# Optimization experiments

Hardware: AMD Instinct MI355X
Metric: run time of the kernel (lower is better)

## Reference

```python
import jax, jax.numpy as jnp
import numpy as np

N, E, C, A, F = 10000, 128000, 128, 10, 8
LDIMS = (1, 3, 5)  # 0e, 1o, 2e spherical-harmonic block sizes
NPATH = len(LDIMS)


def setup_inputs() -> dict:
    key = jax.random.key(0)
    ks = jax.random.split(key, 16)
    rn = lambda k, s, sc=1.0: jax.random.normal(k, s, dtype=jnp.float32) * sc
    inp = {
        "node_attrs": rn(ks[0], (N, A)),
        "node_feats": rn(ks[1], (N, C)),
        "edge_attrs_real": rn(ks[2], (E, 9)),
        "edge_attrs_imag": rn(ks[3], (E, 9)),
        "edge_feats": jax.random.uniform(ks[4], (E, F), dtype=jnp.float32),
        "edge_index": jax.random.randint(ks[5], (2, E), 0, N, dtype=jnp.int32),
        # learned parameters (e3nn 1/sqrt(fan_in) normalization folded into init)
        "W_up": rn(ks[6], (C, C), 1.0 / np.sqrt(C)),            # o3.Linear on 128x0e
        "W_skip": rn(ks[7], (C, A, C), 1.0 / np.sqrt(C * A)),    # FullyConnectedTensorProduct
        "W_mlp1": rn(ks[8], (F, 64), 1.0 / np.sqrt(F)),
        "W_mlp2": rn(ks[9], (64, 64), 1.0 / 8.0),
        "W_mlp3": rn(ks[10], (64, 64), 1.0 / 8.0),
        "W_mlp4": rn(ks[11], (64, NPATH * C), 1.0 / 8.0),        # -> conv_tp.weight_numel = 384
        "W_lin0": rn(ks[12], (C, C), 1.0 / np.sqrt(C)),          # o3.Linear per-l blocks
        "W_lin1": rn(ks[13], (C, C), 1.0 / np.sqrt(C)),
        "W_lin2": rn(ks[14], (C, C), 1.0 / np.sqrt(C)),
    }
    return inp


def _conv_tp(x, y, w):
    """scalar(128x0e) x sh(0e+1o+2e) uvu tensor product with per-edge weights.
    x: [E,C] sender scalars, y: [E,9] edge sh, w: [E,NPATH,C] -> [E, C*9] irreps_mid layout."""
    outs, off = [], 0
    for l, d in enumerate(LDIMS):
        yl = y[:, off:off + d]                      # [E,d]
        off += d
        xw = x * w[:, l]                            # [E,C]
        outs.append((xw[:, :, None] * yl[:, None, :]).reshape(-1, C * d))
    return jnp.concatenate(outs, axis=-1)           # [E, C*(1+3+5)]


def _linear_irreps(m, Ws):
    """o3.Linear mixing channels within each l block. m: [N, C*9] -> [N, C, 9]."""
    outs, off = [], 0
    for l, d in enumerate(LDIMS):
        blk = m[:, off:off + C * d].reshape(-1, C, d)  # [N,C,d]
        off += C * d
        outs.append(jnp.einsum('num,uk->nkm', blk, Ws[l]))
    return jnp.concatenate(outs, axis=-1)              # [N,C,9] (reshape_irreps layout)


def reference(node_attrs, node_feats, edge_attrs_real, edge_attrs_imag, edge_feats,
              edge_index, W_up, W_skip, W_mlp1, W_mlp2, W_mlp3, W_mlp4,
              W_lin0, W_lin1, W_lin2):
    sender, receiver = edge_index[0], edge_index[1]
    # skip connection: FullyConnectedTensorProduct(node_feats 128x0e, node_attrs 10x0e)
    sc = jnp.einsum('nu,nv,uvk->nk', node_feats, node_attrs, W_skip)
    # linear_up
    h = node_feats @ W_up
    # per-edge tensor-product weights from radial MLP (silu hidden layers, linear out)
    t = jax.nn.silu(edge_feats @ W_mlp1)
    t = jax.nn.silu(t @ W_mlp2)
    t = jax.nn.silu(t @ W_mlp3)
    tpw = (t @ W_mlp4).reshape(-1, NPATH, C)
    # gather senders, tensor product for real and imag edge attrs
    xs = h[sender]
    mji_r = _conv_tp(xs, edge_attrs_real, tpw)
    mji_i = _conv_tp(xs, edge_attrs_imag, tpw)
    # scatter-sum to receivers
    msg_r = jax.ops.segment_sum(mji_r, receiver, num_segments=N)
    msg_i = jax.ops.segment_sum(mji_i, receiver, num_segments=N)
    # output linear + reshape_irreps -> [N, C, 9]
    Ws = (W_lin0, W_lin1, W_lin2)
    out_r = _linear_irreps(msg_r, Ws)
    out_i = _linear_irreps(msg_i, Ws)
    return out_r, out_i, sc
```

## Files before the change

kernel.cpp:

```cpp
#include <hip/hip_runtime.h>
#include <hip/hip_bf16.h>

#define N_NODES 10000
#define N_EDGES 128000
#define C_DIM   128

typedef __attribute__((ext_vector_type(8))) short bf16x8;
typedef __attribute__((ext_vector_type(4))) float f32x4;


__device__ __forceinline__ float silu_f(float x) {
  return x / (1.f + __expf(-x));
}

__device__ __forceinline__ unsigned short f2bf(float x) {
  __hip_bfloat16 b = __float2bfloat16(x);
  return *(unsigned short*)&b;
}

__device__ __forceinline__ float bf2f(unsigned short u) {
  __hip_bfloat16 b = *(__hip_bfloat16*)&u;
  return __bfloat162float(b);
}

__device__ __forceinline__ bf16x8 pack8(float4 lo, float4 hi) {
  bf16x8 r;
  r[0] = (short)f2bf(lo.x); r[1] = (short)f2bf(lo.y);
  r[2] = (short)f2bf(lo.z); r[3] = (short)f2bf(lo.w);
  r[4] = (short)f2bf(hi.x); r[5] = (short)f2bf(hi.y);
  r[6] = (short)f2bf(hi.z); r[7] = (short)f2bf(hi.w);
  return r;
}

__global__ void k_hist(const int* __restrict__ recv, int* __restrict__ counts) {
  int e = blockIdx.x * 256 + threadIdx.x;
  if (e < N_EDGES) atomicAdd(&counts[recv[e]], 1);
}

__global__ __launch_bounds__(1024) void k_scan(const int* __restrict__ counts,
                                               int* __restrict__ offsets,
                                               int* __restrict__ cursor) {
  __shared__ int swave[16];
  int tid = threadIdx.x;
  int lane = tid & 63, w = tid >> 6;
  int base = tid * 10;
  int local[10]; int s = 0;
  #pragma unroll
  for (int i = 0; i < 10; i++) {
    int idx = base + i;
    int c = (idx < N_NODES) ? counts[idx] : 0;
    local[i] = s; s += c;
  }
  int inc = s;
  #pragma unroll
  for (int d = 1; d < 64; d <<= 1) {
    int v = __shfl_up(inc, d, 64);
    if (lane >= d) inc += v;
  }
  if (lane == 63) swave[w] = inc;
  __syncthreads();
  if (w == 0) {
    int t = (lane < 16) ? swave[lane] : 0;
    #pragma unroll
    for (int d = 1; d < 16; d <<= 1) {
      int v = __shfl_up(t, d, 64);
      if (lane >= d) t += v;
    }
    if (lane < 16) swave[lane] = t;
  }
  __syncthreads();
  int wpre = (w > 0) ? swave[w - 1] : 0;
  int pre = wpre + (inc - s);
  #pragma unroll
  for (int i = 0; i < 10; i++) {
    int idx = base + i;
    if (idx < N_NODES) { int o = pre + local[i]; offsets[idx] = o; cursor[idx] = o; }
  }
  if (tid == 1023) offsets[N_NODES] = wpre + inc;
}

#define HB_NODES 40
__global__ __launch_bounds__(256) void k_fat1(
    const int* __restrict__ recv, const int* __restrict__ send,
    const float* __restrict__ yr, const float* __restrict__ yi,
    int* __restrict__ cursor, int* __restrict__ order,
    float* __restrict__ y2, int* __restrict__ ss,
    const float* __restrict__ Wskip,
    const float* __restrict__ Wl0, const float* __restrict__ Wl1,
    const float* __restrict__ Wl2,
    const float* __restrict__ W1, const float* __restrict__ W2,
    const float* __restrict__ W3, const float* __restrict__ W4,
    unsigned short* __restrict__ wbT, unsigned short* __restrict__ wlT,
    unsigned short* __restrict__ w1f, unsigned short* __restrict__ w2f,
    unsigned short* __restrict__ w3f, unsigned short* __restrict__ w4f,
    const float* __restrict__ feats, const float* __restrict__ Wup,
    float* __restrict__ h) {
  int b = blockIdx.x;
  int tid = threadIdx.x;
  if (b < 500) {
    int e = b * 256 + tid;
    if (e < N_EDGES) {
      int idx = atomicAdd(&cursor[recv[e]], 1);
      order[idx] = e;
      ss[idx] = send[e];
      float* yy = &y2[(size_t)idx * 20];
      #pragma unroll
      for (int m = 0; m < 9; m++) {
        yy[m] = yr[e * 9 + m];
        yy[9 + m] = yi[e * 9 + m];
      }
      yy[18] = 0.f; yy[19] = 0.f;
    }
  } else if (b < 1468) {
    int idx = (b - 500) * 256 + tid;
    if (idx < 163840) {
      int j = idx >> 7, k = idx & 127;
      int u = j / 10, v = j - u * 10;
      wbT[k * 1280 + v * 128 + u] = f2bf(Wskip[idx]);
    } else if (idx < 212992) {
      int t = idx - 163840;
      int l = t >> 14, r = t & 16383;
      int u = r >> 7, k = r & 127;
      const float* W = (l == 0) ? Wl0 : (l == 1) ? Wl1 : Wl2;
      wlT[(l * 128 + k) * 128 + u] = f2bf(W[r]);
    } else if (idx < 215040) {
      int j = idx - 212992;
      int ct = j >> 9, r = j & 511, n = r >> 5, t = r & 31;
      w1f[j] = (t < 8) ? f2bf(W1[t * 64 + ct * 16 + n]) : (unsigned short)0;
    } else if (idx < 219136) {
      int j = idx - 215040;
      int ctks = j >> 9, r = j & 511, n = r >> 5, t = r & 31;
      int ct = ctks >> 1, ks = ctks & 1;
      w2f[j] = f2bf(W2[(ks * 32 + t) * 64 + ct * 16 + n]);
    } else if (idx < 223232) {
      int j = idx - 219136;
      int ctks = j >> 9, r = j & 511, n = r >> 5, t = r & 31;
      int ct = ctks >> 1, ks = ctks & 1;
      w3f[j] = f2bf(W3[(ks * 32 + t) * 64 + ct * 16 + n]);
    } else if (idx < 247808) {
      int j = idx - 223232;
      int ctks = j >> 9, r = j & 511, n = r >> 5, t = r & 31;
      int ct = ctks >> 1, ks = ctks & 1;
      w4f[j] = f2bf(W4[(ks * 32 + t) * 384 + ct * 16 + n]);
    }
  } else {
    int j = tid & 127;
    int par = tid >> 7;
    int n0 = (b - 1468) * HB_NODES;
    float wreg[128];
    #pragma unroll
    for (int k = 0; k < 128; k++) wreg[k] = Wup[k * 128 + j];
    #pragma unroll 2
    for (int i = par; i < HB_NODES; i += 2) {
      int n = __builtin_amdgcn_readfirstlane(n0 + i);
      const float* fr = &feats[n * 128];
      float acc = 0.f;
      #pragma unroll
      for (int k = 0; k < 128; k++) acc += fr[k] * wreg[k];
      h[n * 128 + j] = acc;
    }
  }
}

__global__ __launch_bounds__(256) void k_fat2(
    const float* __restrict__ f, const float* __restrict__ at,
    const unsigned short* __restrict__ wbT, float* __restrict__ sc_out,
    const float* __restrict__ ef, const int* __restrict__ order,
    const unsigned short* __restrict__ w1f, const unsigned short* __restrict__ w2f,
    const unsigned short* __restrict__ w3f, const unsigned short* __restrict__ w4f,
    unsigned short* __restrict__ tpw) {
  __shared__ unsigned short sA[128][72];
  __shared__ unsigned short sB[128][72];
  int b = blockIdx.x;
  int tid = threadIdx.x;
  int w = tid >> 6, lane = tid & 63;
  int l15 = lane & 15, quad = lane >> 4;

  if (b < 625) {
    int n0 = b * 16;
    int nrow = n0 + l15;
    float4 fA[4][2];
    #pragma unroll
    for (int ks = 0; ks < 4; ks++) {
      fA[ks][0] = *(const float4*)&f[nrow * 128 + ks * 32 + quad * 8];
      fA[ks][1] = *(const float4*)&f[nrow * 128 + ks * 32 + quad * 8 + 4];
    }
    f32x4 acc[2] = {};
    #pragma unroll 1
    for (int c = 0; c < 10; c++) {
      float av = at[nrow * 10 + c];
      bf16x8 af[4];
      #pragma unroll
      for (int ks = 0; ks < 4; ks++) {
        float4 lo = fA[ks][0], hi = fA[ks][1];
        lo.x *= av; lo.y *= av; lo.z *= av; lo.w *= av;
        hi.x *= av; hi.y *= av; hi.z *= av; hi.w *= av;
        af[ks] = pack8(lo, hi);
      }
      #pragma unroll
      for (int kt = 0; kt < 2; kt++) {
        int kcol = w * 32 + kt * 16 + l15;
        #pragma unroll
        for (int ks = 0; ks < 4; ks++) {
          bf16x8 bf = *(const bf16x8*)&wbT[kcol * 1280 + c * 128 + ks * 32 + quad * 8];
          acc[kt] = __builtin_amdgcn_mfma_f32_16x16x32_bf16(af[ks], bf, acc[kt], 0, 0, 0);
        }
      }
    }
    #pragma unroll
    for (int kt = 0; kt < 2; kt++) {
      int kcol = w * 32 + kt * 16 + l15;
      #pragma unroll
      for (int reg = 0; reg < 4; reg++) {
        int n = n0 + quad * 4 + reg;
        __builtin_nontemporal_store(acc[kt][reg], &sc_out[n * 128 + kcol]);
      }
    }
    return;
  }

  int e0 = (b - 625) * 128;
  int fragoff = l15 * 32 + quad * 8;
  int rb = w * 32;

  {
    bf16x8 af[2];
    #pragma unroll
    for (int rt = 0; rt < 2; rt++) {
      bf16x8 a = {};
      if (quad == 0) {
        int pos = e0 + rb + rt * 16 + l15;
        int e = order[pos];
        float4 lo = *(const float4*)&ef[e * 8];
        float4 hi = *(const float4*)&ef[e * 8 + 4];
        a = pack8(lo, hi);
      }
      af[rt] = a;
    }
    f32x4 ac[2][4] = {};
    #pragma unroll
    for (int ct = 0; ct < 4; ct++) {
      bf16x8 bb = *(const bf16x8*)&w1f[ct * 512 + fragoff];
      ac[0][ct] = __builtin_amdgcn_mfma_f32_16x16x32_bf16(af[0], bb, ac[0][ct], 0, 0, 0);
      ac[1][ct] = __builtin_amdgcn_mfma_f32_16x16x32_bf16(af[1], bb, ac[1][ct], 0, 0, 0);
    }
    #pragma unroll
    for (int rt = 0; rt < 2; rt++)
      #pragma unroll
      for (int ct = 0; ct < 4; ct++)
        #pragma unroll
        for (int reg = 0; reg < 4; reg++)
          sA[rb + rt * 16 + quad * 4 + reg][ct * 16 + l15] =
              f2bf(silu_f(ac[rt][ct][reg]));
  }
  asm volatile("" ::: "memory");

  #pragma unroll 1
  for (int layer = 0; layer < 2; layer++) {
    unsigned short (*src)[72] = (layer == 0) ? sA : sB;
    unsigned short (*dst)[72] = (layer == 0) ? sB : sA;
    const unsigned short* wf = (layer == 0) ? w2f : w3f;
    bf16x8 a2[2][2];
    #pragma unroll
    for (int rt = 0; rt < 2; rt++)
      #pragma unroll
      for (int ks = 0; ks < 2; ks++)
        a2[rt][ks] = *(const bf16x8*)&src[rb + rt * 16 + l15][ks * 32 + quad * 8];
    f32x4 ac[2][4] = {};
    #pragma unroll
    for (int ct = 0; ct < 4; ct++)
      #pragma unroll
      for (int ks = 0; ks < 2; ks++) {
        bf16x8 bb = *(const bf16x8*)&wf[(ct * 2 + ks) * 512 + fragoff];
        ac[0][ct] = __builtin_amdgcn_mfma_f32_16x16x32_bf16(a2[0][ks], bb, ac[0][ct], 0, 0, 0);
        ac[1][ct] = __builtin_amdgcn_mfma_f32_16x16x32_bf16(a2[1][ks], bb, ac[1][ct], 0, 0, 0);
      }
    #pragma unroll
    for (int rt = 0; rt < 2; rt++)
      #pragma unroll
      for (int ct = 0; ct < 4; ct++)
        #pragma unroll
        for (int reg = 0; reg < 4; reg++)
          dst[rb + rt * 16 + quad * 4 + reg][ct * 16 + l15] =
              f2bf(silu_f(ac[rt][ct][reg]));
    asm volatile("" ::: "memory");
  }

  bf16x8 a4[2][2];
  #pragma unroll
  for (int rt = 0; rt < 2; rt++)
    #pragma unroll
    for (int ks = 0; ks < 2; ks++)
      a4[rt][ks] = *(const bf16x8*)&sA[rb + rt * 16 + l15][ks * 32 + quad * 8];

  #pragma unroll 1
  for (int ch = 0; ch < 6; ch++) {
    f32x4 ac[2][4] = {};
    #pragma unroll
    for (int ct = 0; ct < 4; ct++)
      #pragma unroll
      for (int ks = 0; ks < 2; ks++) {
        bf16x8 bb = *(const bf16x8*)&w4f[((ch * 4 + ct) * 2 + ks) * 512 + fragoff];
        ac[0][ct] = __builtin_amdgcn_mfma_f32_16x16x32_bf16(a4[0][ks], bb, ac[0][ct], 0, 0, 0);
        ac[1][ct] = __builtin_amdgcn_mfma_f32_16x16x32_bf16(a4[1][ks], bb, ac[1][ct], 0, 0, 0);
      }
    #pragma unroll
    for (int rt = 0; rt < 2; rt++)
      #pragma unroll
      for (int ct = 0; ct < 4; ct++)
        #pragma unroll
        for (int reg = 0; reg < 4; reg++)
          sB[rb + rt * 16 + quad * 4 + reg][ct * 16 + l15] = f2bf(ac[rt][ct][reg]);
    asm volatile("" ::: "memory");
    #pragma unroll
    for (int v = 0; v < 4; v++) {
      int idx = v * 64 + lane;
      int r = idx >> 3, cg = idx & 7;
      uint4 p = *(const uint4*)&sB[rb + r][cg * 8];
      *(uint4*)&tpw[(size_t)(e0 + rb + r) * 384 + ch * 64 + cg * 8] = p;
    }
    asm volatile("" ::: "memory");
  }
}

__device__ __forceinline__ void edge_fma(const float* __restrict__ y2, int pos,
                                         float xv, float t0, float t1, float t2,
                                         float* mr, float* mi) {
  const float* yy = &y2[(size_t)pos * 20];
  float4 v0 = *(const float4*)&yy[0];
  float4 v1 = *(const float4*)&yy[4];
  float4 v2 = *(const float4*)&yy[8];
  float4 v3 = *(const float4*)&yy[12];
  float2 v4 = *(const float2*)&yy[16];
  float xw0 = xv * t0, xw1 = xv * t1, xw2 = xv * t2;
  mr[0] += xw0 * v0.x;
  mr[1] += xw1 * v0.y; mr[2] += xw1 * v0.z; mr[3] += xw1 * v0.w;
  mr[4] += xw2 * v1.x; mr[5] += xw2 * v1.y; mr[6] += xw2 * v1.z;
  mr[7] += xw2 * v1.w; mr[8] += xw2 * v2.x;
  mi[0] += xw0 * v2.y;
  mi[1] += xw1 * v2.z; mi[2] += xw1 * v2.w; mi[3] += xw1 * v3.x;
  mi[4] += xw2 * v3.y; mi[5] += xw2 * v3.z; mi[6] += xw2 * v3.w;
  mi[7] += xw2 * v4.x; mi[8] += xw2 * v4.y;
}

__global__ __launch_bounds__(128, 6) void k_gather(
    const float* __restrict__ h, const unsigned short* __restrict__ tpw,
    const float* __restrict__ y2, const int* __restrict__ ss,
    const int* __restrict__ offsets,
    unsigned short* __restrict__ msg) {
  int u = threadIdx.x;
  int n = blockIdx.x;
  float mr[9] = {}, mi[9] = {};
  int e0 = __builtin_amdgcn_readfirstlane(offsets[n]);
  int e1 = __builtin_amdgcn_readfirstlane(offsets[n + 1]);
  int jj = e0;
  for (; jj + 3 < e1; jj += 4) {
    float xv[4], t0[4], t1[4], t2[4];
    #pragma unroll
    for (int q = 0; q < 4; q++) {
      int pos = jj + q;
      int s = ss[pos];
      const unsigned short* tp = &tpw[(size_t)pos * 384 + u];
      t0[q] = bf2f(__builtin_nontemporal_load(tp));
      t1[q] = bf2f(__builtin_nontemporal_load(tp + 128));
      t2[q] = bf2f(__builtin_nontemporal_load(tp + 256));
      xv[q] = h[s * 128 + u];
    }
    #pragma unroll
    for (int q = 0; q < 4; q++)
      edge_fma(y2, jj + q, xv[q], t0[q], t1[q], t2[q], mr, mi);
  }
  for (; jj < e1; jj++) {
    int s = ss[jj];
    const unsigned short* tp = &tpw[(size_t)jj * 384 + u];
    float t0 = bf2f(__builtin_nontemporal_load(tp));
    float t1 = bf2f(__builtin_nontemporal_load(tp + 128));
    float t2 = bf2f(__builtin_nontemporal_load(tp + 256));
    float xv = h[s * 128 + u];
    edge_fma(y2, jj, xv, t0, t1, t2, mr, mi);
  }
  int g = n >> 3, i = n & 7;
  unsigned short* mg = msg + (size_t)g * 144 * 128;
  mg[(i * 2 + 0) * 128 + u] = f2bf(mr[0]);
  mg[(i * 2 + 1) * 128 + u] = f2bf(mi[0]);
  #pragma unroll
  for (int m = 1; m < 4; m++) {
    mg[(16 + i * 6 + (m - 1)) * 128 + u] = f2bf(mr[m]);
    mg[(16 + i * 6 + 3 + (m - 1)) * 128 + u] = f2bf(mi[m]);
  }
  #pragma unroll
  for (int m = 4; m < 9; m++) {
    mg[(64 + i * 10 + (m - 4)) * 128 + u] = f2bf(mr[m]);
    mg[(64 + i * 10 + 5 + (m - 4)) * 128 + u] = f2bf(mi[m]);
  }
}

#define LIN_ROWPAD 1156
__global__ __launch_bounds__(256) void k_lin(const unsigned short* __restrict__ msg,
                                             const unsigned short* __restrict__ wlT,
                                             float* __restrict__ out) {
  __shared__ float so[2 * 8 * LIN_ROWPAD];
  int tid = threadIdx.x;
  int w = tid >> 6, lane = tid & 63;
  int l15 = lane & 15, quad = lane >> 4;
  int g = blockIdx.x;

  bf16x8 bfr[3][2][4];
  #pragma unroll
  for (int l = 0; l < 3; l++)
    #pragma unroll
    for (int kt = 0; kt < 2; kt++)
      #pragma unroll
      for (int ks = 0; ks < 4; ks++) {
        int ncol = w * 32 + kt * 16 + l15;
        bfr[l][kt][ks] = *(const bf16x8*)&wlT[(l * 128 + ncol) * 128 + ks * 32 + quad * 8];
      }

  const unsigned short* mg = msg + (size_t)g * 144 * 128;

  #pragma unroll
  for (int tile = 0; tile < 9; tile++) {
    const int l = (tile == 0) ? 0 : (tile < 4) ? 1 : 2;
    const int rbase = tile * 16;
    bf16x8 af[4];
    #pragma unroll
    for (int ks = 0; ks < 4; ks++)
      af[ks] = *(const bf16x8*)&mg[(rbase + l15) * 128 + ks * 32 + quad * 8];
    f32x4 acc0 = {}, acc1 = {};
    #pragma unroll
    for (int ks = 0; ks < 4; ks++) {
      acc0 = __builtin_amdgcn_mfma_f32_16x16x32_bf16(af[ks], bfr[l][0][ks], acc0, 0, 0, 0);
      acc1 = __builtin_amdgcn_mfma_f32_16x16x32_bf16(af[ks], bfr[l][1][ks], acc1, 0, 0, 0);
    }
    #pragma unroll
    for (int reg = 0; reg < 4; reg++) {
      int r = rbase + quad * 4 + reg;
      int c, ni, m;
      if (tile == 0) { ni = (r & 15) >> 1; c = r & 1; m = 0; }
      else if (tile < 4) {
        int q = r - 16; ni = q / 6; int rem = q - ni * 6;
        c = rem >= 3; m = 1 + rem - (c ? 3 : 0);
      } else {
        int q = r - 64; ni = q / 10; int rem = q - ni * 10;
        c = rem >= 5; m = 4 + rem - (c ? 5 : 0);
      }
      int k0 = w * 32 + l15;
      float* ob = &so[(c * 8 + ni) * LIN_ROWPAD + m];
      ob[(k0)      * 9] = acc0[reg];
      ob[(k0 + 16) * 9] = acc1[reg];
    }
  }
  __syncthreads();
  #pragma unroll
  for (int v = 0; v < 18; v++) {
    int idx = v * 256 + tid;
    int c = idx / 2304;
    int rem = idx - c * 2304;
    int ni = rem / 288;
    int off4 = rem - ni * 288;
    f32x4 p = *(const f32x4*)&so[(c * 8 + ni) * LIN_ROWPAD + off4 * 4];
    f32x4* dst = (f32x4*)&out[(size_t)c * 11520000 + ((size_t)g * 8 + ni) * 1152 +
                              (size_t)off4 * 4];
    __builtin_nontemporal_store(p, dst);
  }
}

extern "C" void kernel_launch(void* const* d_in, const int* in_sizes, int n_in,
                              void* d_out, int out_size, void* d_ws, size_t ws_size,
                              hipStream_t stream) {
  const float* node_attrs = (const float*)d_in[0];
  const float* node_feats = (const float*)d_in[1];
  const float* ear   = (const float*)d_in[2];
  const float* eai   = (const float*)d_in[3];
  const float* ef    = (const float*)d_in[4];
  const int*   eidx  = (const int*)d_in[5];
  const float* Wup   = (const float*)d_in[6];
  const float* Wskip = (const float*)d_in[7];
  const float* W1    = (const float*)d_in[8];
  const float* W2    = (const float*)d_in[9];
  const float* W3    = (const float*)d_in[10];
  const float* W4    = (const float*)d_in[11];
  const float* Wl0   = (const float*)d_in[12];
  const float* Wl1   = (const float*)d_in[13];
  const float* Wl2   = (const float*)d_in[14];
  float* out = (float*)d_out;

  char* ws = (char*)d_ws;
  float*          h       = (float*)ws;
  unsigned short* tpw     = (unsigned short*)(ws + 5120000);
  unsigned short* msg     = (unsigned short*)(ws + 103424000);
  unsigned short* wlT     = (unsigned short*)(ws + 149504000);
  unsigned short* wbT     = (unsigned short*)(ws + 149602304);
  int*            counts  = (int*)(ws + 149929984);
  int*            offsets = (int*)(ws + 149969984);
  int*            cursor  = (int*)(ws + 150010112);
  int*            order   = (int*)(ws + 150050112);
  unsigned short* w1f     = (unsigned short*)(ws + 150562816);
  unsigned short* w2f     = (unsigned short*)(ws + 150566912);
  unsigned short* w3f     = (unsigned short*)(ws + 150575104);
  unsigned short* w4f     = (unsigned short*)(ws + 150583296);

  float* y2 = (float*)d_out;
  int*   ss = (int*)((char*)d_out + 10240000);

  const int* send = eidx;
  const int* recv = eidx + N_EDGES;

  hipMemsetAsync(counts, 0, N_NODES * sizeof(int), stream);
  k_hist<<<dim3(500), dim3(256), 0, stream>>>(recv, counts);
  k_scan<<<dim3(1), dim3(1024), 0, stream>>>(counts, offsets, cursor);
  k_fat1<<<dim3(1718), dim3(256), 0, stream>>>(
      recv, send, ear, eai, cursor, order, y2, ss,
      Wskip, Wl0, Wl1, Wl2, W1, W2, W3, W4,
      wbT, wlT, w1f, w2f, w3f, w4f,
      node_feats, Wup, h);
  k_fat2<<<dim3(1625), dim3(256), 0, stream>>>(
      node_feats, node_attrs, wbT, out + 2 * 11520000,
      ef, order, w1f, w2f, w3f, w4f, tpw);
  k_gather<<<dim3(10000), dim3(128), 0, stream>>>(h, tpw, y2, ss, offsets, msg);
  k_lin<<<dim3(1250), dim3(256), 0, stream>>>(msg, wlT, out);
  (void)in_sizes; (void)n_in; (void)out_size; (void)ws_size;
}
```

Before: 334.3 us.

## Split h linear into its own kernel, single LDS buffer, nontemporal tpw stores

The Wup node-linear branch, which keeps 128 weights in registers per thread, moves out of the fused k_fat1 into its own k_h kernel. The scatter and weight-prep kernel no longer carries that register pressure, which is meant to raise its occupancy. k_fat2 drops its second shared-memory buffer and reuses sA in place, halving LDS per block to allow more resident blocks. Its tpw output stores become nontemporal to avoid polluting cache. The cost is one extra kernel launch and a serialization point between the split kernels.

```diff
diff --git a/kernel.cpp b/kernel.cpp
--- a/kernel.cpp
+++ b/kernel.cpp
@@ -7,6 +7,7 @@
 
 typedef __attribute__((ext_vector_type(8))) short bf16x8;
 typedef __attribute__((ext_vector_type(4))) float f32x4;
+typedef __attribute__((ext_vector_type(4))) unsigned int u32x4;
 
 
 __device__ __forceinline__ float silu_f(float x) {
@@ -79,8 +80,7 @@
   if (tid == 1023) offsets[N_NODES] = wpre + inc;
 }
 
-#define HB_NODES 40
-__global__ __launch_bounds__(256) void k_fat1(
+__global__ __launch_bounds__(256) void k_sw(
     const int* __restrict__ recv, const int* __restrict__ send,
     const float* __restrict__ yr, const float* __restrict__ yi,
     int* __restrict__ cursor, int* __restrict__ order,
@@ -92,9 +92,7 @@
     const float* __restrict__ W3, const float* __restrict__ W4,
     unsigned short* __restrict__ wbT, unsigned short* __restrict__ wlT,
     unsigned short* __restrict__ w1f, unsigned short* __restrict__ w2f,
-    unsigned short* __restrict__ w3f, unsigned short* __restrict__ w4f,
-    const float* __restrict__ feats, const float* __restrict__ Wup,
-    float* __restrict__ h) {
+    unsigned short* __restrict__ w3f, unsigned short* __restrict__ w4f) {
   int b = blockIdx.x;
   int tid = threadIdx.x;
   if (b < 500) {
@@ -111,7 +109,7 @@
       }
       yy[18] = 0.f; yy[19] = 0.f;
     }
-  } else if (b < 1468) {
+  } else {
     int idx = (b - 500) * 256 + tid;
     if (idx < 163840) {
       int j = idx >> 7, k = idx & 127;
@@ -143,22 +141,28 @@
       int ct = ctks >> 1, ks = ctks & 1;
       w4f[j] = f2bf(W4[(ks * 32 + t) * 384 + ct * 16 + n]);
     }
-  } else {
-    int j = tid & 127;
-    int par = tid >> 7;
-    int n0 = (b - 1468) * HB_NODES;
-    float wreg[128];
-    #pragma unroll
-    for (int k = 0; k < 128; k++) wreg[k] = Wup[k * 128 + j];
-    #pragma unroll 2
-    for (int i = par; i < HB_NODES; i += 2) {
-      int n = __builtin_amdgcn_readfirstlane(n0 + i);
-      const float* fr = &feats[n * 128];
-      float acc = 0.f;
-      #pragma unroll
-      for (int k = 0; k < 128; k++) acc += fr[k] * wreg[k];
-      h[n * 128 + j] = acc;
-    }
+  }
+}
+
+#define HB_NODES 40
+__global__ __launch_bounds__(256) void k_h(const float* __restrict__ feats,
+                                           const float* __restrict__ Wup,
+                                           float* __restrict__ h) {
+  int tid = threadIdx.x;
+  int j = tid & 127;
+  int par = tid >> 7;
+  int n0 = blockIdx.x * HB_NODES;
+  float wreg[128];
+  #pragma unroll
+  for (int k = 0; k < 128; k++) wreg[k] = Wup[k * 128 + j];
+  #pragma unroll 2
+  for (int i = par; i < HB_NODES; i += 2) {
+    int n = __builtin_amdgcn_readfirstlane(n0 + i);
+    const float* fr = &feats[n * 128];
+    float acc = 0.f;
+    #pragma unroll
+    for (int k = 0; k < 128; k++) acc += fr[k] * wreg[k];
+    h[n * 128 + j] = acc;
   }
 }
 
@@ -170,7 +174,6 @@
     const unsigned short* __restrict__ w3f, const unsigned short* __restrict__ w4f,
     unsigned short* __restrict__ tpw) {
   __shared__ unsigned short sA[128][72];
-  __shared__ unsigned short sB[128][72];
   int b = blockIdx.x;
   int tid = threadIdx.x;
   int w = tid >> 6, lane = tid & 63;
@@ -257,15 +260,13 @@
 
   #pragma unroll 1
   for (int layer = 0; layer < 2; layer++) {
-    unsigned short (*src)[72] = (layer == 0) ? sA : sB;
-    unsigned short (*dst)[72] = (layer == 0) ? sB : sA;
     const unsigned short* wf = (layer == 0) ? w2f : w3f;
     bf16x8 a2[2][2];
     #pragma unroll
     for (int rt = 0; rt < 2; rt++)
       #pragma unroll
       for (int ks = 0; ks < 2; ks++)
-        a2[rt][ks] = *(const bf16x8*)&src[rb + rt * 16 + l15][ks * 32 + quad * 8];
+        a2[rt][ks] = *(const bf16x8*)&sA[rb + rt * 16 + l15][ks * 32 + quad * 8];
     f32x4 ac[2][4] = {};
     #pragma unroll
     for (int ct = 0; ct < 4; ct++)
@@ -281,7 +282,7 @@
       for (int ct = 0; ct < 4; ct++)
         #pragma unroll
         for (int reg = 0; reg < 4; reg++)
-          dst[rb + rt * 16 + quad * 4 + reg][ct * 16 + l15] =
+          sA[rb + rt * 16 + quad * 4 + reg][ct * 16 + l15] =
               f2bf(silu_f(ac[rt][ct][reg]));
     asm volatile("" ::: "memory");
   }
@@ -292,6 +293,7 @@
     #pragma unroll
     for (int ks = 0; ks < 2; ks++)
       a4[rt][ks] = *(const bf16x8*)&sA[rb + rt * 16 + l15][ks * 32 + quad * 8];
+  asm volatile("" ::: "memory");
 
   #pragma unroll 1
   for (int ch = 0; ch < 6; ch++) {
@@ -310,14 +312,15 @@
       for (int ct = 0; ct < 4; ct++)
         #pragma unroll
         for (int reg = 0; reg < 4; reg++)
-          sB[rb + rt * 16 + quad * 4 + reg][ct * 16 + l15] = f2bf(ac[rt][ct][reg]);
+          sA[rb + rt * 16 + quad * 4 + reg][ct * 16 + l15] = f2bf(ac[rt][ct][reg]);
     asm volatile("" ::: "memory");
     #pragma unroll
     for (int v = 0; v < 4; v++) {
       int idx = v * 64 + lane;
       int r = idx >> 3, cg = idx & 7;
-      uint4 p = *(const uint4*)&sB[rb + r][cg * 8];
-      *(uint4*)&tpw[(size_t)(e0 + rb + r) * 384 + ch * 64 + cg * 8] = p;
+      u32x4 p = *(const u32x4*)&sA[rb + r][cg * 8];
+      __builtin_nontemporal_store(
+          p, (u32x4*)&tpw[(size_t)(e0 + rb + r) * 384 + ch * 64 + cg * 8]);
     }
     asm volatile("" ::: "memory");
   }
@@ -509,11 +512,11 @@
   hipMemsetAsync(counts, 0, N_NODES * sizeof(int), stream);
   k_hist<<<dim3(500), dim3(256), 0, stream>>>(recv, counts);
   k_scan<<<dim3(1), dim3(1024), 0, stream>>>(counts, offsets, cursor);
-  k_fat1<<<dim3(1718), dim3(256), 0, stream>>>(
+  k_sw<<<dim3(1468), dim3(256), 0, stream>>>(
       recv, send, ear, eai, cursor, order, y2, ss,
       Wskip, Wl0, Wl1, Wl2, W1, W2, W3, W4,
-      wbT, wlT, w1f, w2f, w3f, w4f,
-      node_feats, Wup, h);
+      wbT, wlT, w1f, w2f, w3f, w4f);
+  k_h<<<dim3(250), dim3(256), 0, stream>>>(node_feats, Wup, h);
   k_fat2<<<dim3(1625), dim3(256), 0, stream>>>(
       node_feats, node_attrs, wbT, out + 2 * 11520000,
       ef, order, w1f, w2f, w3f, w4f, tpw);
```

Result: no change. 336.9 us (+0.8%).
